# Optimization experiments

Measured on AMD Instinct MI355X. Metric: run time of the kernel, lower is better.

Reference implementation:

```python
import jax, jax.numpy as jnp
import numpy as np

N = 100000
E = 1600000
IN_DIM, HID, NCLS = 512, 64, 16


def setup_inputs() -> dict:
    key = jax.random.key(0)
    ks = jax.random.split(key, 6)
    x = jax.random.normal(ks[0], (N, IN_DIM), dtype=jnp.float32)
    edge_index = jax.random.randint(ks[1], (2, E), 0, N, dtype=jnp.int32)
    edge_weight = jax.random.uniform(ks[2], (E,), dtype=jnp.float32)
    W1 = jax.random.normal(ks[3], (IN_DIM, HID), dtype=jnp.float32) / np.sqrt(IN_DIM)
    b1 = jnp.zeros((HID,), dtype=jnp.float32)
    W2 = jax.random.normal(ks[4], (HID, NCLS), dtype=jnp.float32) / np.sqrt(HID)
    b2 = jnp.zeros((NCLS,), dtype=jnp.float32)
    return {"x": x, "edge_index": edge_index, "edge_weight": edge_weight,
            "W1": W1, "b1": b1, "W2": W2, "b2": b2}


def _gcn_norm(edge_index, edge_weight, num_nodes):
    # PyG GCNConv: add self-loops (weight 1), symmetric deg^-1/2 normalization.
    loop = jnp.arange(num_nodes, dtype=edge_index.dtype)
    src = jnp.concatenate([edge_index[0], loop])
    dst = jnp.concatenate([edge_index[1], loop])
    w = jnp.concatenate([edge_weight, jnp.ones((num_nodes,), edge_weight.dtype)])
    deg = jax.ops.segment_sum(w, dst, num_segments=num_nodes)  # degree at target
    dis = jnp.where(deg > 0, jax.lax.rsqrt(jnp.where(deg > 0, deg, 1.0)), 0.0)
    norm = dis[src] * w * dis[dst]
    return src, dst, norm


def _gcn_layer(x, src, dst, norm, W, b):
    h = x @ W                                   # [N, out]
    msg = h[src] * norm[:, None]                # gather + scale  [E+N, out]
    out = jax.ops.segment_sum(msg, dst, num_segments=x.shape[0])
    return out + b


def reference(x, edge_index, edge_weight, W1, b1, W2, b2):
    src, dst, norm = _gcn_norm(edge_index, edge_weight, x.shape[0])
    h = _gcn_layer(x, src, dst, norm, W1, b1)
    h = jax.nn.relu(h)
    # F.dropout in eval mode is identity (reference assumes inference).
    h = _gcn_layer(h, src, dst, norm, W2, b2)
    return jax.nn.log_softmax(h, axis=-1)
```

## Files before the change

kernel.cpp:

```cpp
#include <hip/hip_runtime.h>
#include <hip/hip_bf16.h>

#define N_NODES 100000
#define N_EDGES 1600000
#define IN_DIM 512
#define HID 64
#define NCLS 16
#define NB ((N_NODES + 1023) / 1024)

typedef __attribute__((ext_vector_type(8))) short bf16x8;
typedef __attribute__((ext_vector_type(8))) unsigned short ushort8;
typedef __attribute__((ext_vector_type(4))) float f32x4;

static __device__ __forceinline__ unsigned short f2bf(float f) {
    union { float f; unsigned int u; } v; v.f = f;
    unsigned int u = v.u;
    unsigned int r = (u + 0x7fffu + ((u >> 16) & 1u)) >> 16;
    return (unsigned short)r;
}
static __device__ __forceinline__ float bf2f(unsigned short u) {
    union { unsigned int i; float f; } v; v.i = ((unsigned int)u) << 16; return v.f;
}


__global__ void k_init(int* cnt) {
    int i = blockIdx.x * 256 + threadIdx.x;
    if (i < N_NODES) cnt[i] = 0;
}

__global__ void k_pass1(const int* __restrict__ dst, int* cnt, int* __restrict__ li) {
    int e = blockIdx.x * 256 + threadIdx.x;
    if (e < N_EDGES) li[e] = atomicAdd(&cnt[dst[e]], 1);
}

__global__ void k_scan1(const int* __restrict__ cnt, int* ptr, int* bsum) {
    __shared__ int s[256];
    int t = threadIdx.x;
    int i0 = blockIdx.x * 1024 + t * 4;
    int c[4];
#pragma unroll
    for (int j = 0; j < 4; j++) c[j] = (i0 + j < N_NODES) ? cnt[i0 + j] : 0;
    int sum4 = c[0] + c[1] + c[2] + c[3];
    s[t] = sum4;
    __syncthreads();
    int v = sum4;
    for (int off = 1; off < 256; off <<= 1) {
        int add = (t >= off) ? s[t - off] : 0;
        __syncthreads();
        v += add;
        s[t] = v;
        __syncthreads();
    }
    int run = v - sum4;
#pragma unroll
    for (int j = 0; j < 4; j++) {
        if (i0 + j < N_NODES) ptr[i0 + j] = run;
        run += c[j];
    }
    if (t == 255) bsum[blockIdx.x] = v;
}

__global__ void k_scan2(int* bsum, int* ptr) {
    __shared__ int s[128];
    int t = threadIdx.x;
    int val = (t < NB) ? bsum[t] : 0;
    s[t] = val;
    __syncthreads();
    int v = val;
    for (int off = 1; off < 128; off <<= 1) {
        int add = (t >= off) ? s[t - off] : 0;
        __syncthreads();
        v += add;
        s[t] = v;
        __syncthreads();
    }
    if (t < NB) bsum[t] = v - val;
    if (t == 0) ptr[N_NODES] = N_EDGES;
}

__global__ void k_scan3(int* ptr, const int* __restrict__ bsum) {
    int t = threadIdx.x;
    int i0 = blockIdx.x * 1024 + t * 4;
    int add = bsum[blockIdx.x];
#pragma unroll
    for (int j = 0; j < 4; j++)
        if (i0 + j < N_NODES) ptr[i0 + j] += add;
}

__global__ void k_pass2(const int* __restrict__ src, const int* __restrict__ dst,
                        const float* __restrict__ w, const int* __restrict__ ptr,
                        const int* __restrict__ li,
                        int* __restrict__ csr_src, float* __restrict__ csr_w) {
    int e = blockIdx.x * 256 + threadIdx.x;
    if (e < N_EDGES) {
        int p = ptr[dst[e]] + li[e];
        csr_src[p] = src[e];
        csr_w[p] = w[e];
    }
}

__global__ void k_degsum(const int* __restrict__ ptr, const float* __restrict__ csr_w,
                         float* __restrict__ dis) {
    int v = blockIdx.x * 256 + threadIdx.x;
    if (v < N_NODES) {
        int p0 = ptr[v], p1 = ptr[v + 1];
        float s = 1.0f;
        for (int p = p0; p < p1; p++) s += csr_w[p];
        dis[v] = rsqrtf(s);
    }
}


__global__ void k_prep_w1(const float* __restrict__ W1, unsigned short* __restrict__ wt) {
    int t = blockIdx.x * 256 + threadIdx.x;
    if (t < HID * IN_DIM) {
        int n = t >> 9, k = t & 511;
        wt[t] = f2bf(W1[(size_t)k * HID + n]);
    }
}


#define LDK 72

__global__ __launch_bounds__(256) void k_gemm1(const float* __restrict__ x,
                                               const unsigned short* __restrict__ wt,
                                               const float* __restrict__ dis,
                                               unsigned short* __restrict__ h1s) {
    __shared__ unsigned short xs[64][LDK];
    __shared__ unsigned short ws[64][LDK];

    int t = threadIdx.x;
    int row0 = blockIdx.x * 64;
    int wave = t >> 6, lane = t & 63;
    int lm = lane & 15, quad = lane >> 4;

    f32x4 acc[4];
#pragma unroll
    for (int nt = 0; nt < 4; nt++) acc[nt] = (f32x4)(0.f);

    for (int k0 = 0; k0 < IN_DIM; k0 += 64) {
        __syncthreads();
        {
            int c8 = (t & 7) * 8;
#pragma unroll
            for (int h = 0; h < 2; h++) {
                int r = (t >> 3) + h * 32;
                int gr = row0 + r;
                if (gr >= N_NODES) gr = N_NODES - 1;
                const float* xp = x + (size_t)gr * IN_DIM + k0 + c8;
                float4 v0 = *(const float4*)xp;
                float4 v1 = *(const float4*)(xp + 4);
                ushort8 pk;
                pk.s0 = f2bf(v0.x); pk.s1 = f2bf(v0.y); pk.s2 = f2bf(v0.z); pk.s3 = f2bf(v0.w);
                pk.s4 = f2bf(v1.x); pk.s5 = f2bf(v1.y); pk.s6 = f2bf(v1.z); pk.s7 = f2bf(v1.w);
                *(ushort8*)&xs[r][c8] = pk;
            }
        }
        {
            int n = t >> 2, kc = (t & 3) * 16;
            const unsigned short* wp = wt + (size_t)n * IN_DIM + k0 + kc;
            *(ushort8*)&ws[n][kc]     = *(const ushort8*)wp;
            *(ushort8*)&ws[n][kc + 8] = *(const ushort8*)(wp + 8);
        }
        __syncthreads();
#pragma unroll
        for (int kk = 0; kk < 64; kk += 32) {
            bf16x8 afrag = *(bf16x8*)&xs[wave * 16 + lm][kk + quad * 8];
#pragma unroll
            for (int nt = 0; nt < 4; nt++) {
                bf16x8 bfrag = *(bf16x8*)&ws[nt * 16 + lm][kk + quad * 8];
                acc[nt] = __builtin_amdgcn_mfma_f32_16x16x32_bf16(afrag, bfrag, acc[nt], 0, 0, 0);
            }
        }
    }
#pragma unroll
    for (int i = 0; i < 4; i++) {
        int gr = row0 + wave * 16 + quad * 4 + i;
        if (gr < N_NODES) {
            float dv = dis[gr];
#pragma unroll
            for (int nt = 0; nt < 4; nt++)
                h1s[(size_t)gr * HID + nt * 16 + lm] = f2bf(dv * acc[nt][i]);
        }
    }
}


__global__ __launch_bounds__(256) void k_agg1(const unsigned short* __restrict__ h1s,
                                              const int* __restrict__ ptr,
                                              const int* __restrict__ csr_src,
                                              const float* __restrict__ csr_w,
                                              const float* __restrict__ dis,
                                              const float* __restrict__ b1,
                                              unsigned short* __restrict__ a1s) {
    int t = blockIdx.x * 256 + threadIdx.x;
    int v = t >> 4, c = t & 15;
    if (v >= N_NODES) return;
    int p0 = ptr[v], p1 = ptr[v + 1];

    float a0 = 0.f, a1v = 0.f, a2 = 0.f, a3 = 0.f;
    for (int base = p0; base < p1; base += 4) {
#pragma unroll
        for (int u = 0; u < 4; u++) {
            int idx = base + u;
            bool valid = idx < p1;
            int s = valid ? csr_src[idx] : v;
            float wgt = valid ? csr_w[idx] : 0.f;
            ushort4 g = *(const ushort4*)&h1s[(size_t)s * HID + c * 4];
            a0 += wgt * bf2f(g.x);
            a1v += wgt * bf2f(g.y);
            a2 += wgt * bf2f(g.z);
            a3 += wgt * bf2f(g.w);
        }
    }
    float dv = dis[v];
    ushort4 sv = *(const ushort4*)&h1s[(size_t)v * HID + c * 4];
    float4 bv = *(const float4*)&b1[c * 4];
    float r0 = dv * (a0 + bf2f(sv.x)) + bv.x;
    float r1 = dv * (a1v + bf2f(sv.y)) + bv.y;
    float r2 = dv * (a2 + bf2f(sv.z)) + bv.z;
    float r3 = dv * (a3 + bf2f(sv.w)) + bv.w;
    ushort4 o;
    o.x = f2bf(r0 > 0.f ? r0 : 0.f);
    o.y = f2bf(r1 > 0.f ? r1 : 0.f);
    o.z = f2bf(r2 > 0.f ? r2 : 0.f);
    o.w = f2bf(r3 > 0.f ? r3 : 0.f);
    *(ushort4*)&a1s[(size_t)v * HID + c * 4] = o;
}


__global__ __launch_bounds__(256) void k_gemm2(const unsigned short* __restrict__ a1s,
                                               const float* __restrict__ W2,
                                               const float* __restrict__ dis,
                                               unsigned short* __restrict__ h2s) {
    __shared__ float ws[HID * NCLS];
    for (int i = threadIdx.x; i < HID * NCLS; i += 256) ws[i] = W2[i];
    __syncthreads();
    int t = blockIdx.x * 256 + threadIdx.x;
    int v = t >> 4, cc = t & 15;
    if (v >= N_NODES) return;
    const unsigned short* row = a1s + (size_t)v * HID;
    float acc = 0.f;
#pragma unroll
    for (int k = 0; k < HID; k += 4) {
        ushort4 av = *(const ushort4*)(row + k);
        acc = fmaf(bf2f(av.x), ws[(k + 0) * NCLS + cc], acc);
        acc = fmaf(bf2f(av.y), ws[(k + 1) * NCLS + cc], acc);
        acc = fmaf(bf2f(av.z), ws[(k + 2) * NCLS + cc], acc);
        acc = fmaf(bf2f(av.w), ws[(k + 3) * NCLS + cc], acc);
    }
    h2s[(size_t)v * NCLS + cc] = f2bf(dis[v] * acc);
}


__global__ __launch_bounds__(256) void k_agg2(const unsigned short* __restrict__ h2s,
                                              const int* __restrict__ ptr,
                                              const int* __restrict__ csr_src,
                                              const float* __restrict__ csr_w,
                                              const float* __restrict__ dis,
                                              const float* __restrict__ b2,
                                              float* __restrict__ out) {
    int t = blockIdx.x * 256 + threadIdx.x;
    int v = t >> 4, c = t & 15;
    if (v >= N_NODES) return;
    int p0 = ptr[v], p1 = ptr[v + 1];

    float acc = 0.f;
    for (int base = p0; base < p1; base += 4) {
#pragma unroll
        for (int u = 0; u < 4; u++) {
            int idx = base + u;
            bool valid = idx < p1;
            int s = valid ? csr_src[idx] : v;
            float wgt = valid ? csr_w[idx] : 0.f;
            acc += wgt * bf2f(h2s[(size_t)s * NCLS + c]);
        }
    }
    float dv = dis[v];
    float z = dv * (acc + bf2f(h2s[(size_t)v * NCLS + c])) + b2[c];

    float mx = z;
#pragma unroll
    for (int off = 8; off >= 1; off >>= 1) mx = fmaxf(mx, __shfl_xor(mx, off, 16));
    float e = expf(z - mx);
    float s = e;
#pragma unroll
    for (int off = 8; off >= 1; off >>= 1) s += __shfl_xor(s, off, 16);
    out[(size_t)v * NCLS + c] = z - mx - logf(s);
}


extern "C" void kernel_launch(void* const* d_in, const int* in_sizes, int n_in,
                              void* d_out, int out_size, void* d_ws, size_t ws_size,
                              hipStream_t stream) {
    const float* x  = (const float*)d_in[0];
    const int*   ei = (const int*)d_in[1];
    const float* w  = (const float*)d_in[2];
    const float* W1 = (const float*)d_in[3];
    const float* b1 = (const float*)d_in[4];
    const float* W2 = (const float*)d_in[5];
    const float* b2 = (const float*)d_in[6];
    const int* src = ei;
    const int* dst = ei + N_EDGES;

    char* wsb = (char*)d_ws;
    size_t off = 0;
    auto alloc = [&](size_t bytes) {
        void* p = wsb + off;
        off += (bytes + 255) & ~(size_t)255;
        return p;
    };
    int*   cnt   = (int*)  alloc((size_t)N_NODES * 4);
    int*   li    = (int*)  alloc((size_t)N_EDGES * 4);
    int*   ptr   = (int*)  alloc((size_t)(N_NODES + 1) * 4);
    int*   bsum  = (int*)  alloc((size_t)NB * 4);
    int*   csr_s = (int*)  alloc((size_t)N_EDGES * 4);
    float* csr_w = (float*)alloc((size_t)N_EDGES * 4);
    float* dis   = (float*)alloc((size_t)N_NODES * 4);
    unsigned short* h1s = (unsigned short*)alloc((size_t)N_NODES * HID * 2);
    unsigned short* a1s = (unsigned short*)alloc((size_t)N_NODES * HID * 2);
    unsigned short* h2s = (unsigned short*)alloc((size_t)N_NODES * NCLS * 2);
    unsigned short* wt  = (unsigned short*)alloc((size_t)HID * IN_DIM * 2);

    float* outp = (float*)d_out;

    k_init   <<<(N_NODES + 255) / 256, 256, 0, stream>>>(cnt);
    k_pass1  <<<(N_EDGES + 255) / 256, 256, 0, stream>>>(dst, cnt, li);
    k_scan1  <<<NB, 256, 0, stream>>>(cnt, ptr, bsum);
    k_scan2  <<<1, 128, 0, stream>>>(bsum, ptr);
    k_scan3  <<<NB, 256, 0, stream>>>(ptr, bsum);
    k_pass2  <<<(N_EDGES + 255) / 256, 256, 0, stream>>>(src, dst, w, ptr, li, csr_s, csr_w);
    k_degsum <<<(N_NODES + 255) / 256, 256, 0, stream>>>(ptr, csr_w, dis);
    k_prep_w1<<<(HID * IN_DIM + 255) / 256, 256, 0, stream>>>(W1, wt);
    k_gemm1  <<<(N_NODES + 63) / 64, 256, 0, stream>>>(x, wt, dis, h1s);
    k_agg1   <<<(N_NODES * 16 + 255) / 256, 256, 0, stream>>>(h1s, ptr, csr_s, csr_w, dis, b1, a1s);
    k_gemm2  <<<(N_NODES * 16 + 255) / 256, 256, 0, stream>>>(a1s, W2, dis, h2s);
    k_agg2   <<<(N_NODES * 16 + 255) / 256, 256, 0, stream>>>(h2s, ptr, csr_s, csr_w, dis, b2, outp);
}
```

Before: 553.7 us.

## Overlap edge counting with GEMM1 in one interleaved launch and pack CSR

GEMM1 no longer depends on the degree normalization. It is merged into one launch with the edge-count atomic pass, interleaving one GEMM block with four counting blocks, so the memory-bound x read overlaps the atomic scatter. The source-side deg^-1/2 scaling moves into the aggregation loops, which read dis[src] per edge, and the self-loop term uses dis^2. CSR source and weight are packed into one int2 array, the aggregation unroll goes from 4 to 8, and the init and W1-prep kernels are merged. The cost is an extra random gather of dis per edge in both aggregation passes.

```diff
diff --git a/kernel.cpp b/kernel.cpp
--- a/kernel.cpp
+++ b/kernel.cpp
@@ -8,6 +8,10 @@
 #define NCLS 16
 #define NB ((N_NODES + 1023) / 1024)
 
+#define GEMM_BLOCKS ((N_NODES + 63) / 64)
+#define PASS_BLOCKS ((N_EDGES + 255) / 256)
+#define FUSED_GRID (GEMM_BLOCKS + PASS_BLOCKS)
+
 typedef __attribute__((ext_vector_type(8))) short bf16x8;
 typedef __attribute__((ext_vector_type(8))) unsigned short ushort8;
 typedef __attribute__((ext_vector_type(4))) float f32x4;
@@ -21,17 +25,101 @@
 static __device__ __forceinline__ float bf2f(unsigned short u) {
     union { unsigned int i; float f; } v; v.i = ((unsigned int)u) << 16; return v.f;
 }
-
-
-__global__ void k_init(int* cnt) {
-    int i = blockIdx.x * 256 + threadIdx.x;
-    if (i < N_NODES) cnt[i] = 0;
-}
-
-__global__ void k_pass1(const int* __restrict__ dst, int* cnt, int* __restrict__ li) {
-    int e = blockIdx.x * 256 + threadIdx.x;
-    if (e < N_EDGES) li[e] = atomicAdd(&cnt[dst[e]], 1);
-}
+static __device__ __forceinline__ unsigned int f2bf2u(float a, float b) {
+    union { __hip_bfloat162 h; unsigned int u; } cv;
+    cv.h = __float22bfloat162_rn(make_float2(a, b));
+    return cv.u;
+}
+
+
+__global__ void k_setup(int* cnt, const float* __restrict__ W1,
+                        unsigned short* __restrict__ wt) {
+    int t = blockIdx.x * 256 + threadIdx.x;
+    if (t < N_NODES) cnt[t] = 0;
+    int j = t - N_NODES;
+    if (j >= 0 && j < HID * IN_DIM) {
+        int n = j >> 9, k = j & 511;
+        wt[j] = f2bf(W1[(size_t)k * HID + n]);
+    }
+}
+
+
+#define LDK 72
+
+__global__ __launch_bounds__(256) void k_fused(const int* __restrict__ dst,
+                                               int* cnt, int* __restrict__ li,
+                                               const float* __restrict__ x,
+                                               const unsigned short* __restrict__ wt,
+                                               unsigned short* __restrict__ h1s) {
+    __shared__ unsigned short xs[64][LDK];
+    __shared__ unsigned short ws[64][LDK];
+
+    int b = blockIdx.x;
+    int q = b / 5, r = b % 5;
+    if (r != 0) {
+        int pid = q * 4 + r - 1;
+        int e = pid * 256 + threadIdx.x;
+        if (e < N_EDGES) li[e] = atomicAdd(&cnt[dst[e]], 1);
+        return;
+    }
+    int gid = q;
+    int t = threadIdx.x;
+    int row0 = gid * 64;
+    int wave = t >> 6, lane = t & 63;
+    int lm = lane & 15, quad = lane >> 4;
+
+    f32x4 acc[4];
+#pragma unroll
+    for (int nt = 0; nt < 4; nt++) acc[nt] = (f32x4)(0.f);
+
+    for (int k0 = 0; k0 < IN_DIM; k0 += 64) {
+        __syncthreads();
+        {
+            int c8 = (t & 7) * 8;
+#pragma unroll
+            for (int h = 0; h < 2; h++) {
+                int rr = (t >> 3) + h * 32;
+                int gr = row0 + rr;
+                if (gr >= N_NODES) gr = N_NODES - 1;
+                const float* xp = x + (size_t)gr * IN_DIM + k0 + c8;
+                float4 v0 = *(const float4*)xp;
+                float4 v1 = *(const float4*)(xp + 4);
+                union { ushort8 s; unsigned int u[4]; } pk;
+                pk.u[0] = f2bf2u(v0.x, v0.y);
+                pk.u[1] = f2bf2u(v0.z, v0.w);
+                pk.u[2] = f2bf2u(v1.x, v1.y);
+                pk.u[3] = f2bf2u(v1.z, v1.w);
+                *(ushort8*)&xs[rr][c8] = pk.s;
+            }
+        }
+        {
+            int n = t >> 2, kc = (t & 3) * 16;
+            const unsigned short* wp = wt + (size_t)n * IN_DIM + k0 + kc;
+            *(ushort8*)&ws[n][kc]     = *(const ushort8*)wp;
+            *(ushort8*)&ws[n][kc + 8] = *(const ushort8*)(wp + 8);
+        }
+        __syncthreads();
+#pragma unroll
+        for (int kk = 0; kk < 64; kk += 32) {
+            bf16x8 afrag = *(bf16x8*)&xs[wave * 16 + lm][kk + quad * 8];
+#pragma unroll
+            for (int nt = 0; nt < 4; nt++) {
+                bf16x8 bfrag = *(bf16x8*)&ws[nt * 16 + lm][kk + quad * 8];
+                acc[nt] = __builtin_amdgcn_mfma_f32_16x16x32_bf16(afrag, bfrag, acc[nt], 0, 0, 0);
+            }
+        }
+    }
+#pragma unroll
+    for (int i = 0; i < 4; i++) {
+        int gr = row0 + wave * 16 + quad * 4 + i;
+        if (gr < N_NODES) {
+#pragma unroll
+            for (int nt = 0; nt < 4; nt++)
+                h1s[(size_t)gr * HID + nt * 16 + lm] = f2bf(acc[nt][i]);
+        }
+    }
+}
+
 
 __global__ void k_scan1(const int* __restrict__ cnt, int* ptr, int* bsum) {
     __shared__ int s[256];
@@ -87,109 +175,33 @@
         if (i0 + j < N_NODES) ptr[i0 + j] += add;
 }
 
+
 __global__ void k_pass2(const int* __restrict__ src, const int* __restrict__ dst,
                         const float* __restrict__ w, const int* __restrict__ ptr,
-                        const int* __restrict__ li,
-                        int* __restrict__ csr_src, float* __restrict__ csr_w) {
+                        const int* __restrict__ li, int2* __restrict__ csr) {
     int e = blockIdx.x * 256 + threadIdx.x;
     if (e < N_EDGES) {
         int p = ptr[dst[e]] + li[e];
-        csr_src[p] = src[e];
-        csr_w[p] = w[e];
-    }
-}
-
-__global__ void k_degsum(const int* __restrict__ ptr, const float* __restrict__ csr_w,
+        csr[p] = make_int2(src[e], __float_as_int(w[e]));
+    }
+}
+
+
+__global__ void k_degsum(const int* __restrict__ ptr, const int2* __restrict__ csr,
                          float* __restrict__ dis) {
     int v = blockIdx.x * 256 + threadIdx.x;
     if (v < N_NODES) {
         int p0 = ptr[v], p1 = ptr[v + 1];
         float s = 1.0f;
-        for (int p = p0; p < p1; p++) s += csr_w[p];
+        for (int p = p0; p < p1; p++) s += __int_as_float(csr[p].y);
         dis[v] = rsqrtf(s);
-    }
-}
-
-
-__global__ void k_prep_w1(const float* __restrict__ W1, unsigned short* __restrict__ wt) {
-    int t = blockIdx.x * 256 + threadIdx.x;
-    if (t < HID * IN_DIM) {
-        int n = t >> 9, k = t & 511;
-        wt[t] = f2bf(W1[(size_t)k * HID + n]);
-    }
-}
-
-
-#define LDK 72
-
-__global__ __launch_bounds__(256) void k_gemm1(const float* __restrict__ x,
-                                               const unsigned short* __restrict__ wt,
-                                               const float* __restrict__ dis,
-                                               unsigned short* __restrict__ h1s) {
-    __shared__ unsigned short xs[64][LDK];
-    __shared__ unsigned short ws[64][LDK];
-
-    int t = threadIdx.x;
-    int row0 = blockIdx.x * 64;
-    int wave = t >> 6, lane = t & 63;
-    int lm = lane & 15, quad = lane >> 4;
-
-    f32x4 acc[4];
-#pragma unroll
-    for (int nt = 0; nt < 4; nt++) acc[nt] = (f32x4)(0.f);
-
-    for (int k0 = 0; k0 < IN_DIM; k0 += 64) {
-        __syncthreads();
-        {
-            int c8 = (t & 7) * 8;
-#pragma unroll
-            for (int h = 0; h < 2; h++) {
-                int r = (t >> 3) + h * 32;
-                int gr = row0 + r;
-                if (gr >= N_NODES) gr = N_NODES - 1;
-                const float* xp = x + (size_t)gr * IN_DIM + k0 + c8;
-                float4 v0 = *(const float4*)xp;
-                float4 v1 = *(const float4*)(xp + 4);
-                ushort8 pk;
-                pk.s0 = f2bf(v0.x); pk.s1 = f2bf(v0.y); pk.s2 = f2bf(v0.z); pk.s3 = f2bf(v0.w);
-                pk.s4 = f2bf(v1.x); pk.s5 = f2bf(v1.y); pk.s6 = f2bf(v1.z); pk.s7 = f2bf(v1.w);
-                *(ushort8*)&xs[r][c8] = pk;
-            }
-        }
-        {
-            int n = t >> 2, kc = (t & 3) * 16;
-            const unsigned short* wp = wt + (size_t)n * IN_DIM + k0 + kc;
-            *(ushort8*)&ws[n][kc]     = *(const ushort8*)wp;
-            *(ushort8*)&ws[n][kc + 8] = *(const ushort8*)(wp + 8);
-        }
-        __syncthreads();
-#pragma unroll
-        for (int kk = 0; kk < 64; kk += 32) {
-            bf16x8 afrag = *(bf16x8*)&xs[wave * 16 + lm][kk + quad * 8];
-#pragma unroll
-            for (int nt = 0; nt < 4; nt++) {
-                bf16x8 bfrag = *(bf16x8*)&ws[nt * 16 + lm][kk + quad * 8];
-                acc[nt] = __builtin_amdgcn_mfma_f32_16x16x32_bf16(afrag, bfrag, acc[nt], 0, 0, 0);
-            }
-        }
-    }
-#pragma unroll
-    for (int i = 0; i < 4; i++) {
-        int gr = row0 + wave * 16 + quad * 4 + i;
-        if (gr < N_NODES) {
-            float dv = dis[gr];
-#pragma unroll
-            for (int nt = 0; nt < 4; nt++)
-                h1s[(size_t)gr * HID + nt * 16 + lm] = f2bf(dv * acc[nt][i]);
-        }
     }
 }
 
 
 __global__ __launch_bounds__(256) void k_agg1(const unsigned short* __restrict__ h1s,
                                               const int* __restrict__ ptr,
-                                              const int* __restrict__ csr_src,
-                                              const float* __restrict__ csr_w,
+                                              const int2* __restrict__ csr,
                                               const float* __restrict__ dis,
                                               const float* __restrict__ b1,
                                               unsigned short* __restrict__ a1s) {
@@ -199,13 +211,14 @@
     int p0 = ptr[v], p1 = ptr[v + 1];
 
     float a0 = 0.f, a1v = 0.f, a2 = 0.f, a3 = 0.f;
-    for (int base = p0; base < p1; base += 4) {
-#pragma unroll
-        for (int u = 0; u < 4; u++) {
+    for (int base = p0; base < p1; base += 8) {
+#pragma unroll
+        for (int u = 0; u < 8; u++) {
             int idx = base + u;
             bool valid = idx < p1;
-            int s = valid ? csr_src[idx] : v;
-            float wgt = valid ? csr_w[idx] : 0.f;
+            int2 cw = valid ? csr[idx] : make_int2(v, 0);
+            int s = cw.x;
+            float wgt = __int_as_float(cw.y) * dis[s];
             ushort4 g = *(const ushort4*)&h1s[(size_t)s * HID + c * 4];
             a0 += wgt * bf2f(g.x);
             a1v += wgt * bf2f(g.y);
@@ -213,13 +226,13 @@
             a3 += wgt * bf2f(g.w);
         }
     }
-    float dv = dis[v];
+    float dv = dis[v], dvv = dv * dv;
     ushort4 sv = *(const ushort4*)&h1s[(size_t)v * HID + c * 4];
     float4 bv = *(const float4*)&b1[c * 4];
-    float r0 = dv * (a0 + bf2f(sv.x)) + bv.x;
-    float r1 = dv * (a1v + bf2f(sv.y)) + bv.y;
-    float r2 = dv * (a2 + bf2f(sv.z)) + bv.z;
-    float r3 = dv * (a3 + bf2f(sv.w)) + bv.w;
+    float r0 = dv * a0 + dvv * bf2f(sv.x) + bv.x;
+    float r1 = dv * a1v + dvv * bf2f(sv.y) + bv.y;
+    float r2 = dv * a2 + dvv * bf2f(sv.z) + bv.z;
+    float r3 = dv * a3 + dvv * bf2f(sv.w) + bv.w;
     ushort4 o;
     o.x = f2bf(r0 > 0.f ? r0 : 0.f);
     o.y = f2bf(r1 > 0.f ? r1 : 0.f);
@@ -231,7 +244,6 @@
 
 __global__ __launch_bounds__(256) void k_gemm2(const unsigned short* __restrict__ a1s,
                                                const float* __restrict__ W2,
-                                               const float* __restrict__ dis,
                                                unsigned short* __restrict__ h2s) {
     __shared__ float ws[HID * NCLS];
     for (int i = threadIdx.x; i < HID * NCLS; i += 256) ws[i] = W2[i];
@@ -249,14 +261,13 @@
         acc = fmaf(bf2f(av.z), ws[(k + 2) * NCLS + cc], acc);
         acc = fmaf(bf2f(av.w), ws[(k + 3) * NCLS + cc], acc);
     }
-    h2s[(size_t)v * NCLS + cc] = f2bf(dis[v] * acc);
+    h2s[(size_t)v * NCLS + cc] = f2bf(acc);
 }
 
 
 __global__ __launch_bounds__(256) void k_agg2(const unsigned short* __restrict__ h2s,
                                               const int* __restrict__ ptr,
-                                              const int* __restrict__ csr_src,
-                                              const float* __restrict__ csr_w,
+                                              const int2* __restrict__ csr,
                                               const float* __restrict__ dis,
                                               const float* __restrict__ b2,
                                               float* __restrict__ out) {
@@ -266,18 +277,19 @@
     int p0 = ptr[v], p1 = ptr[v + 1];
 
     float acc = 0.f;
-    for (int base = p0; base < p1; base += 4) {
-#pragma unroll
-        for (int u = 0; u < 4; u++) {
+    for (int base = p0; base < p1; base += 8) {
+#pragma unroll
+        for (int u = 0; u < 8; u++) {
             int idx = base + u;
             bool valid = idx < p1;
-            int s = valid ? csr_src[idx] : v;
-            float wgt = valid ? csr_w[idx] : 0.f;
+            int2 cw = valid ? csr[idx] : make_int2(v, 0);
+            int s = cw.x;
+            float wgt = __int_as_float(cw.y) * dis[s];
             acc += wgt * bf2f(h2s[(size_t)s * NCLS + c]);
         }
     }
-    float dv = dis[v];
-    float z = dv * (acc + bf2f(h2s[(size_t)v * NCLS + c])) + b2[c];
+    float dv = dis[v], dvv = dv * dv;
+    float z = dv * acc + dvv * bf2f(h2s[(size_t)v * NCLS + c]) + b2[c];
 
     float mx = z;
 #pragma unroll
@@ -314,8 +326,7 @@
     int*   li    = (int*)  alloc((size_t)N_EDGES * 4);
     int*   ptr   = (int*)  alloc((size_t)(N_NODES + 1) * 4);
     int*   bsum  = (int*)  alloc((size_t)NB * 4);
-    int*   csr_s = (int*)  alloc((size_t)N_EDGES * 4);
-    float* csr_w = (float*)alloc((size_t)N_EDGES * 4);
+    int2*  csr   = (int2*) alloc((size_t)N_EDGES * 8);
     float* dis   = (float*)alloc((size_t)N_NODES * 4);
     unsigned short* h1s = (unsigned short*)alloc((size_t)N_NODES * HID * 2);
     unsigned short* a1s = (unsigned short*)alloc((size_t)N_NODES * HID * 2);
@@ -324,16 +335,14 @@
 
     float* outp = (float*)d_out;
 
-    k_init   <<<(N_NODES + 255) / 256, 256, 0, stream>>>(cnt);
-    k_pass1  <<<(N_EDGES + 255) / 256, 256, 0, stream>>>(dst, cnt, li);
+    k_setup  <<<(N_NODES + HID * IN_DIM + 255) / 256, 256, 0, stream>>>(cnt, W1, wt);
+    k_fused  <<<FUSED_GRID, 256, 0, stream>>>(dst, cnt, li, x, wt, h1s);
     k_scan1  <<<NB, 256, 0, stream>>>(cnt, ptr, bsum);
     k_scan2  <<<1, 128, 0, stream>>>(bsum, ptr);
     k_scan3  <<<NB, 256, 0, stream>>>(ptr, bsum);
-    k_pass2  <<<(N_EDGES + 255) / 256, 256, 0, stream>>>(src, dst, w, ptr, li, csr_s, csr_w);
-    k_degsum <<<(N_NODES + 255) / 256, 256, 0, stream>>>(ptr, csr_w, dis);
-    k_prep_w1<<<(HID * IN_DIM + 255) / 256, 256, 0, stream>>>(W1, wt);
-    k_gemm1  <<<(N_NODES + 63) / 64, 256, 0, stream>>>(x, wt, dis, h1s);
-    k_agg1   <<<(N_NODES * 16 + 255) / 256, 256, 0, stream>>>(h1s, ptr, csr_s, csr_w, dis, b1, a1s);
-    k_gemm2  <<<(N_NODES * 16 + 255) / 256, 256, 0, stream>>>(a1s, W2, dis, h2s);
-    k_agg2   <<<(N_NODES * 16 + 255) / 256, 256, 0, stream>>>(h2s, ptr, csr_s, csr_w, dis, b2, outp);
-}
+    k_pass2  <<<PASS_BLOCKS, 256, 0, stream>>>(src, dst, w, ptr, li, csr);
+    k_degsum <<<(N_NODES + 255) / 256, 256, 0, stream>>>(ptr, csr, dis);
+    k_agg1   <<<(N_NODES * 16 + 255) / 256, 256, 0, stream>>>(h1s, ptr, csr, dis, b1, a1s);
+    k_gemm2  <<<(N_NODES * 16 + 255) / 256, 256, 0, stream>>>(a1s, W2, h2s);
+    k_agg2   <<<(N_NODES * 16 + 255) / 256, 256, 0, stream>>>(h2s, ptr, csr, dis, b2, outp);
+}
```

Result: faster. 491.9 us (-11.2%).
